# Optimization experiments

Measured on AMD Instinct MI355X. Metric: run time of the kernel, lower is better.

Reference implementation:

```python
import jax, jax.numpy as jnp
import numpy as np

HEADS = 4
DIM_HEAD = 128


def setup_inputs() -> dict:
    key = jax.random.key(0)
    k1, k2, k3, k4 = jax.random.split(key, 4)
    B, C, H, W = 8, 256, 64, 64
    hidden = HEADS * DIM_HEAD  # 512
    x = jax.random.normal(k1, (B, C, H, W), dtype=jnp.float32)
    # 1x1 convs are just channel matmuls; store kernels as [out_ch, in_ch]
    w_qkv = jax.random.normal(k2, (3 * hidden, C), dtype=jnp.float32) * 0.05
    w_out = jax.random.normal(k3, (C, hidden), dtype=jnp.float32) * 0.05
    b_out = jax.random.normal(k4, (C,), dtype=jnp.float32) * 0.05
    return {"x": x, "w_qkv": w_qkv, "w_out": w_out, "b_out": b_out}


def reference(x, w_qkv, w_out, b_out):
    B, C, H, W = x.shape
    n = H * W
    # to_qkv: 1x1 conv without bias == channel matmul
    qkv = jnp.einsum('bchw,oc->bohw', x, w_qkv)  # [B, 3*heads*dim_head, H, W]
    qkv = qkv.reshape(B, 3, HEADS, DIM_HEAD, n)  # 'b (qkv heads c) h w -> b qkv heads c n'
    q, k, v = qkv[:, 0], qkv[:, 1], qkv[:, 2]    # each [B, heads, dim_head, n]
    k = jax.nn.softmax(k, axis=-1)               # softmax over spatial positions
    context = jnp.einsum('bhdn,bhen->bhde', k, v)   # [B, heads, d, e]
    out = jnp.einsum('bhde,bhdn->bhen', context, q)  # [B, heads, e, n]
    out = out.reshape(B, HEADS * DIM_HEAD, H, W)
    # to_out: 1x1 conv with bias
    return jnp.einsum('bchw,oc->bohw', out, w_out) + b_out[None, :, None, None]
```

## Files before the change

kernel.cpp:

```cpp
#include <hip/hip_runtime.h>
#include <stdint.h>


using frag8 = __attribute__((ext_vector_type(8))) short;
using f32x4 = __attribute__((ext_vector_type(4))) float;

__device__ __forceinline__ unsigned short f2bf(float f) {
    union { float f; unsigned int u; } c; c.f = f;
    unsigned int u = c.u;
    return (unsigned short)((u + 0x7FFFu + ((u >> 16) & 1u)) >> 16);
}

__device__ __forceinline__ void gl_lds16(const void* g, void* l) {
    __builtin_amdgcn_global_load_lds(
        (const __attribute__((address_space(1))) unsigned int*)g,
        (__attribute__((address_space(3))) unsigned int*)l, 16, 0, 0);
}

__global__ __launch_bounds__(256) void k0_weights(
    const float* __restrict__ w_qkv, const float* __restrict__ w_out,
    unsigned short* __restrict__ wkvb, unsigned short* __restrict__ woutb,
    unsigned short* __restrict__ wqT)
{
    __shared__ float T[64][65];
    const int blk = blockIdx.x;
    const int tid = threadIdx.x;
    if (blk < 256) {
        const int idx = (blk * 256 + tid) * 4;
        float4 v = *(const float4*)(w_qkv + 512 * 256 + idx);
        ushort4 o;
        o.x = f2bf(v.x); o.y = f2bf(v.y); o.z = f2bf(v.z); o.w = f2bf(v.w);
        *(ushort4*)(wkvb + idx) = o;
    } else if (blk < 384) {
        const int idx = ((blk - 256) * 256 + tid) * 4;
        float4 v = *(const float4*)(w_out + idx);
        ushort4 o;
        o.x = f2bf(v.x); o.y = f2bf(v.y); o.z = f2bf(v.z); o.w = f2bf(v.w);
        *(ushort4*)(woutb + idx) = o;
    } else {
        const int t = blk - 384;
        const int j0 = (t >> 2) * 64, c0 = (t & 3) * 64;
        const int r = tid >> 4, cc = (tid & 15) * 4;
        #pragma unroll
        for (int p = 0; p < 4; ++p) {
            float4 v = *(const float4*)(w_qkv + (j0 + r + p * 16) * 256 + c0 + cc);
            T[r + p * 16][cc + 0] = v.x; T[r + p * 16][cc + 1] = v.y;
            T[r + p * 16][cc + 2] = v.z; T[r + p * 16][cc + 3] = v.w;
        }
        __syncthreads();
        const int c = tid >> 2, jj = (tid & 3) * 16;
        #pragma unroll
        for (int g = 0; g < 4; ++g) {
            ushort4 o;
            o.x = f2bf(T[jj + g * 4 + 0][c]);
            o.y = f2bf(T[jj + g * 4 + 1][c]);
            o.z = f2bf(T[jj + g * 4 + 2][c]);
            o.w = f2bf(T[jj + g * 4 + 3][c]);
            *(ushort4*)(wqT + (c0 + c) * 512 + j0 + jj + g * 4) = o;
        }
    }
}

__global__ __launch_bounds__(256) void k0_xt(
    const float* __restrict__ x, unsigned short* __restrict__ xbT)
{
    __shared__ float T[64][65];
    const int tid = threadIdx.x;
    const int n0 = blockIdx.x * 64, c0 = blockIdx.y * 64, b = blockIdx.z;
    const float* xb = x + (size_t)b * 1048576;
    const int cr = tid >> 4, nc = (tid & 15) * 4;
    #pragma unroll
    for (int p = 0; p < 4; ++p) {
        float4 v = *(const float4*)(xb + (size_t)(c0 + cr + p * 16) * 4096 + n0 + nc);
        T[cr + p * 16][nc + 0] = v.x; T[cr + p * 16][nc + 1] = v.y;
        T[cr + p * 16][nc + 2] = v.z; T[cr + p * 16][nc + 3] = v.w;
    }
    __syncthreads();
    const int n = tid >> 2, cc = (tid & 3) * 16;
    unsigned short* dst = xbT + (size_t)b * 1048576 + (size_t)(n0 + n) * 256 + c0 + cc;
    #pragma unroll
    for (int g = 0; g < 4; ++g) {
        ushort4 o;
        o.x = f2bf(T[cc + g * 4 + 0][n]);
        o.y = f2bf(T[cc + g * 4 + 1][n]);
        o.z = f2bf(T[cc + g * 4 + 2][n]);
        o.w = f2bf(T[cc + g * 4 + 3][n]);
        *(ushort4*)(dst + g * 4) = o;
    }
}

template<int MODE>
__global__ __launch_bounds__(256) void mfma_bt(
    const unsigned short* __restrict__ A0, int lda,
    const unsigned short* __restrict__ B0, int ldb,
    void* __restrict__ C0, int ldc,
    const float* __restrict__ bias, int Kp,
    unsigned long long sAz, unsigned long long sBz, unsigned long long sCz)
{
    __shared__ unsigned short As[128 * 32];
    __shared__ unsigned short Bs[128 * 32];
    const int tid  = threadIdx.x;
    const int w    = tid >> 6, lane = tid & 63;
    const int quad = lane >> 4, l16 = lane & 15;
    const int wm = (w >> 1) * 64, wn = (w & 1) * 64;
    const int z = blockIdx.z;

    const unsigned short* A;
    const unsigned short* B;
    int m0, n0;
    if constexpr (MODE == 3) {
        m0 = blockIdx.y * 128; n0 = 0;
        A = A0 + (unsigned long long)(z & 3) * 128ull + (unsigned long long)m0 * lda;
        B = B0 + (unsigned long long)z * 16384ull;
    } else {
        m0 = blockIdx.y * 128; n0 = blockIdx.x * 128;
        A = A0 + sAz * z + (unsigned long long)m0 * lda;
        B = B0 + sBz * z + (unsigned long long)n0 * ldb;
    }

    const int c0 = w * 128 + lane, c1 = c0 + 64;
    const int r0 = c0 >> 2, g0 = ((c0 & 3) ^ ((r0 >> 1) & 3)) * 8;
    const int r1 = c1 >> 2, g1 = ((c1 & 3) ^ ((r1 >> 1) & 3)) * 8;
    const unsigned short* gA0 = A + (unsigned long long)r0 * lda + g0;
    const unsigned short* gA1 = A + (unsigned long long)r1 * lda + g1;
    const unsigned short* gB0 = B + (unsigned long long)r0 * ldb + g0;
    const unsigned short* gB1 = B + (unsigned long long)r1 * ldb + g1;
    unsigned short* lA0 = As + w * 1024;
    unsigned short* lA1 = As + w * 1024 + 512;
    unsigned short* lB0 = Bs + w * 1024;
    unsigned short* lB1 = Bs + w * 1024 + 512;

    f32x4 acc[4][4] = {};

    for (int k0 = 0; k0 < Kp; k0 += 32) {
        gl_lds16(gA0 + k0, lA0);
        gl_lds16(gA1 + k0, lA1);
        gl_lds16(gB0 + k0, lB0);
        gl_lds16(gB1 + k0, lB1);
        __syncthreads();
        frag8 a[4], b[4];
        #pragma unroll
        for (int t = 0; t < 4; ++t) {
            const int ra = wm + t * 16 + l16;
            const int rb = wn + t * 16 + l16;
            a[t] = *(const frag8*)(As + ra * 32 + ((quad ^ ((ra >> 1) & 3)) << 3));
            b[t] = *(const frag8*)(Bs + rb * 32 + ((quad ^ ((rb >> 1) & 3)) << 3));
        }
        #pragma unroll
        for (int mt = 0; mt < 4; ++mt)
            #pragma unroll
            for (int nt = 0; nt < 4; ++nt)
                acc[mt][nt] = __builtin_amdgcn_mfma_f32_16x16x32_bf16(
                    a[mt], b[nt], acc[mt][nt], 0, 0, 0);
        __syncthreads();
    }

    if constexpr (MODE == 0 || MODE == 3) {
        unsigned short* C;
        if constexpr (MODE == 0)
            C = (unsigned short*)C0 + sCz * z + (unsigned long long)m0 * ldc + n0;
        else
            C = (unsigned short*)C0 + (unsigned long long)(z >> 2) * 131072ull
              + (unsigned long long)(z & 3) * 128ull + (unsigned long long)m0 * ldc;
        #pragma unroll
        for (int mt = 0; mt < 4; ++mt) {
            const int row = wm + mt * 16 + quad * 4;
            #pragma unroll
            for (int nt = 0; nt < 4; ++nt) {
                const int col = wn + nt * 16 + l16;
                #pragma unroll
                for (int r = 0; r < 4; ++r)
                    C[(unsigned long long)(row + r) * ldc + col] = f2bf(acc[mt][nt][r]);
            }
        }
    } else {
        float* C = (float*)C0 + sCz * z + (unsigned long long)m0 * ldc + n0;
        const float* bp = bias + m0;
        #pragma unroll
        for (int mt = 0; mt < 4; ++mt) {
            const int row = wm + mt * 16 + quad * 4;
            #pragma unroll
            for (int nt = 0; nt < 4; ++nt) {
                const int col = wn + nt * 16 + l16;
                #pragma unroll
                for (int r = 0; r < 4; ++r)
                    C[(unsigned long long)(row + r) * ldc + col] = acc[mt][nt][r] + bp[row + r];
            }
        }
    }
}

__global__ __launch_bounds__(256) void k13_ctx(
    const unsigned short* __restrict__ wkvb,
    const unsigned short* __restrict__ xbT,
    float* __restrict__ ctx, float* __restrict__ rowsum)
{
    __shared__ unsigned short As[128 * 32];
    __shared__ unsigned short Bs[128 * 32];
    __shared__ unsigned short Kt[128 * 128];
    __shared__ unsigned short Vt[128 * 128];
    const int tid  = threadIdx.x;
    const int w    = tid >> 6, lane = tid & 63;
    const int quad = lane >> 4, l16 = lane & 15;
    const int wm = (w >> 1) * 64, wn = (w & 1) * 64;
    const int s = blockIdx.x, h = blockIdx.y, b = blockIdx.z;

    const unsigned short* Wk = wkvb + (size_t)(h * 128) * 256;
    const unsigned short* Wv = wkvb + (size_t)(512 + h * 128) * 256;
    const unsigned short* Xb = xbT + (size_t)b * 1048576;

    const int c0 = w * 128 + lane, c1 = c0 + 64;
    const int r0 = c0 >> 2, g0 = ((c0 & 3) ^ ((r0 >> 1) & 3)) * 8;
    const int r1 = c1 >> 2, g1 = ((c1 & 3) ^ ((r1 >> 1) & 3)) * 8;
    unsigned short* lA0 = As + w * 1024;
    unsigned short* lA1 = As + w * 1024 + 512;
    unsigned short* lB0 = Bs + w * 1024;
    unsigned short* lB1 = Bs + w * 1024 + 512;

    float rsum[4][4] = {};
    f32x4 ctxa[4][4] = {};

    for (int ch = 0; ch < 2; ++ch) {
        const unsigned short* X0 = Xb + (size_t)(blockIdx.x * 256 + ch * 128) * 256;

        #pragma unroll 1
        for (int g = 0; g < 2; ++g) {
            const unsigned short* Wg = g ? Wv : Wk;
            f32x4 acc[4][4] = {};
            for (int k0 = 0; k0 < 256; k0 += 32) {
                gl_lds16(Wg + (size_t)r0 * 256 + g0 + k0, lA0);
                gl_lds16(Wg + (size_t)r1 * 256 + g1 + k0, lA1);
                gl_lds16(X0 + (size_t)r0 * 256 + g0 + k0, lB0);
                gl_lds16(X0 + (size_t)r1 * 256 + g1 + k0, lB1);
                __syncthreads();
                frag8 a[4], bb[4];
                #pragma unroll
                for (int t = 0; t < 4; ++t) {
                    const int ra = wm + t * 16 + l16;
                    const int rb = wn + t * 16 + l16;
                    a[t]  = *(const frag8*)(As + ra * 32 + ((quad ^ ((ra >> 1) & 3)) << 3));
                    bb[t] = *(const frag8*)(Bs + rb * 32 + ((quad ^ ((rb >> 1) & 3)) << 3));
                }
                #pragma unroll
                for (int mt = 0; mt < 4; ++mt)
                    #pragma unroll
                    for (int nt = 0; nt < 4; ++nt)
                        acc[mt][nt] = __builtin_amdgcn_mfma_f32_16x16x32_bf16(
                            a[mt], bb[nt], acc[mt][nt], 0, 0, 0);
                __syncthreads();
            }
            unsigned short* T = g ? Vt : Kt;
            if (g == 0) {
                #pragma unroll
                for (int mt = 0; mt < 4; ++mt) {
                    const int row = wm + mt * 16 + quad * 4;
                    #pragma unroll
                    for (int nt = 0; nt < 4; ++nt) {
                        const int col = wn + nt * 16 + l16;
                        #pragma unroll
                        for (int r = 0; r < 4; ++r) {
                            float e = __expf(acc[mt][nt][r]);
                            rsum[mt][r] += e;
                            T[((row + r) * 128 + col) ^ (((row + r) & 7) << 3)] = f2bf(e);
                        }
                    }
                }
            } else {
                #pragma unroll
                for (int mt = 0; mt < 4; ++mt) {
                    const int row = wm + mt * 16 + quad * 4;
                    #pragma unroll
                    for (int nt = 0; nt < 4; ++nt) {
                        const int col = wn + nt * 16 + l16;
                        #pragma unroll
                        for (int r = 0; r < 4; ++r)
                            T[((row + r) * 128 + col) ^ (((row + r) & 7) << 3)] =
                                f2bf(acc[mt][nt][r]);
                    }
                }
            }
        }
        __syncthreads();

        #pragma unroll
        for (int kk = 0; kk < 4; ++kk) {
            frag8 a[4], bb[4];
            #pragma unroll
            for (int t = 0; t < 4; ++t) {
                const int ra = wm + t * 16 + l16;
                const int rb = wn + t * 16 + l16;
                a[t]  = *(const frag8*)(Kt + ((ra * 128 + kk * 32 + quad * 8) ^ ((ra & 7) << 3)));
                bb[t] = *(const frag8*)(Vt + ((rb * 128 + kk * 32 + quad * 8) ^ ((rb & 7) << 3)));
            }
            #pragma unroll
            for (int mt = 0; mt < 4; ++mt)
                #pragma unroll
                for (int nt = 0; nt < 4; ++nt)
                    ctxa[mt][nt] = __builtin_amdgcn_mfma_f32_16x16x32_bf16(
                        a[mt], bb[nt], ctxa[mt][nt], 0, 0, 0);
        }
        __syncthreads();
    }

    float* cp = ctx + (size_t)(b * 4 + h) * 16384ull;
    #pragma unroll
    for (int mt = 0; mt < 4; ++mt) {
        const int row = wm + mt * 16 + quad * 4;
        #pragma unroll
        for (int nt = 0; nt < 4; ++nt) {
            const int col = wn + nt * 16 + l16;
            #pragma unroll
            for (int r = 0; r < 4; ++r)
                atomicAdd(cp + (row + r) * 128 + col, ctxa[mt][nt][r]);
        }
    }
    float* rs = rowsum + b * 512 + h * 128;
    #pragma unroll
    for (int mt = 0; mt < 4; ++mt) {
        const int row = wm + mt * 16 + quad * 4;
        #pragma unroll
        for (int r = 0; r < 4; ++r) {
            float v = rsum[mt][r];
            v += __shfl_xor(v, 1, 64);
            v += __shfl_xor(v, 2, 64);
            v += __shfl_xor(v, 4, 64);
            v += __shfl_xor(v, 8, 64);
            if (l16 == 0) atomicAdd(rs + row + r, v);
        }
    }
}

__global__ __launch_bounds__(256) void k3_scale(
    const float* __restrict__ ctx, const float* __restrict__ rowsum,
    unsigned short* __restrict__ ctxb)
{
    const int idx = (blockIdx.x * 256 + threadIdx.x) * 4;
    const float inv = 1.0f / rowsum[idx >> 7];
    float4 t = *(const float4*)(ctx + idx);
    ushort4 o;
    o.x = f2bf(t.x * inv); o.y = f2bf(t.y * inv);
    o.z = f2bf(t.z * inv); o.w = f2bf(t.w * inv);
    *(ushort4*)(ctxb + idx) = o;
}

extern "C" void kernel_launch(void* const* d_in, const int* in_sizes, int n_in,
                              void* d_out, int out_size, void* d_ws, size_t ws_size,
                              hipStream_t stream) {
    (void)in_sizes; (void)n_in; (void)out_size; (void)ws_size;
    const float* x     = (const float*)d_in[0];
    const float* w_qkv = (const float*)d_in[1];
    const float* w_out = (const float*)d_in[2];
    const float* b_out = (const float*)d_in[3];
    float* out = (float*)d_out;

    char* ws = (char*)d_ws;
    unsigned short* xbT    = (unsigned short*)ws;
    unsigned short* wkvb   = (unsigned short*)(ws + 16777216);
    unsigned short* woutb  = (unsigned short*)(ws + 17301504);
    unsigned short* wqT    = (unsigned short*)(ws + 17563648);
    float*          ctx    = (float*)(ws + 17825792);
    float*          rowsum = (float*)(ws + 19922944);
    unsigned short* ctxb   = (unsigned short*)(ws + 19939328);
    unsigned short* Mb     = (unsigned short*)(ws + 20987904);
    unsigned short* Nb     = (unsigned short*)(ws + 23085056);

    hipMemsetAsync(ws + 17825792, 0, 2097152 + 16384, stream);

    k0_weights<<<dim3(416), 256, 0, stream>>>(w_qkv, w_out, wkvb, woutb, wqT);
    k0_xt<<<dim3(64, 4, 8), 256, 0, stream>>>(x, xbT);
    k13_ctx<<<dim3(16, 4, 8), 256, 0, stream>>>(wkvb, xbT, ctx, rowsum);
    k3_scale<<<dim3(512), 256, 0, stream>>>(ctx, rowsum, ctxb);
    mfma_bt<3><<<dim3(1, 2, 32), 256, 0, stream>>>(
        woutb, 512, ctxb, 128, Mb, 512, nullptr, 128,
        0ull, 0ull, 0ull);
    mfma_bt<0><<<dim3(2, 2, 8), 256, 0, stream>>>(
        Mb, 512, wqT, 512, Nb, 256, nullptr, 512,
        131072ull, 0ull, 65536ull);
    mfma_bt<1><<<dim3(32, 2, 8), 256, 0, stream>>>(
        Nb, 256, xbT, 256, out, 4096, b_out, 256,
        65536ull, 1048576ull, 1048576ull);
}
```

Measured before the change: 200.5 us.

## Double-buffer K/V projection loads and fuse weight and x prep kernels

Merges the x-transpose and weight-conversion kernels into one launch to cut launch overhead. In the context kernel, K and V projections are computed together sharing the X fragment, with double-buffered global-to-LDS loads overlapped with MFMA through explicit waitcnt and barriers. LDS is unified into one 64KB buffer reused for staging and K/V tiles, and launch bounds request two blocks per CU. This raises register pressure because two accumulator sets are live at once, and it relies on hand-placed vmcnt counts being correct.

```diff
diff --git a/kernel.cpp b/kernel.cpp
--- a/kernel.cpp
+++ b/kernel.cpp
@@ -17,14 +17,40 @@
         (__attribute__((address_space(3))) unsigned int*)l, 16, 0, 0);
 }
 
-__global__ __launch_bounds__(256) void k0_weights(
-    const float* __restrict__ w_qkv, const float* __restrict__ w_out,
-    unsigned short* __restrict__ wkvb, unsigned short* __restrict__ woutb,
-    unsigned short* __restrict__ wqT)
+__global__ __launch_bounds__(256) void k0_prep(
+    const float* __restrict__ x, const float* __restrict__ w_qkv,
+    const float* __restrict__ w_out,
+    unsigned short* __restrict__ xbT, unsigned short* __restrict__ wkvb,
+    unsigned short* __restrict__ woutb, unsigned short* __restrict__ wqT)
 {
     __shared__ float T[64][65];
-    const int blk = blockIdx.x;
     const int tid = threadIdx.x;
+    const int blk0 = blockIdx.x;
+    if (blk0 < 2048) {
+        const int n0 = (blk0 & 63) * 64, c0 = ((blk0 >> 6) & 3) * 64, b = blk0 >> 8;
+        const float* xb = x + (size_t)b * 1048576;
+        const int cr = tid >> 4, nc = (tid & 15) * 4;
+        #pragma unroll
+        for (int p = 0; p < 4; ++p) {
+            float4 v = *(const float4*)(xb + (size_t)(c0 + cr + p * 16) * 4096 + n0 + nc);
+            T[cr + p * 16][nc + 0] = v.x; T[cr + p * 16][nc + 1] = v.y;
+            T[cr + p * 16][nc + 2] = v.z; T[cr + p * 16][nc + 3] = v.w;
+        }
+        __syncthreads();
+        const int n = tid >> 2, cc = (tid & 3) * 16;
+        unsigned short* dst = xbT + (size_t)b * 1048576 + (size_t)(n0 + n) * 256 + c0 + cc;
+        #pragma unroll
+        for (int g = 0; g < 4; ++g) {
+            ushort4 o;
+            o.x = f2bf(T[cc + g * 4 + 0][n]);
+            o.y = f2bf(T[cc + g * 4 + 1][n]);
+            o.z = f2bf(T[cc + g * 4 + 2][n]);
+            o.w = f2bf(T[cc + g * 4 + 3][n]);
+            *(ushort4*)(dst + g * 4) = o;
+        }
+        return;
+    }
+    const int blk = blk0 - 2048;
     if (blk < 256) {
         const int idx = (blk * 256 + tid) * 4;
         float4 v = *(const float4*)(w_qkv + 512 * 256 + idx);
@@ -61,34 +87,6 @@
     }
 }
 
-__global__ __launch_bounds__(256) void k0_xt(
-    const float* __restrict__ x, unsigned short* __restrict__ xbT)
-{
-    __shared__ float T[64][65];
-    const int tid = threadIdx.x;
-    const int n0 = blockIdx.x * 64, c0 = blockIdx.y * 64, b = blockIdx.z;
-    const float* xb = x + (size_t)b * 1048576;
-    const int cr = tid >> 4, nc = (tid & 15) * 4;
-    #pragma unroll
-    for (int p = 0; p < 4; ++p) {
-        float4 v = *(const float4*)(xb + (size_t)(c0 + cr + p * 16) * 4096 + n0 + nc);
-        T[cr + p * 16][nc + 0] = v.x; T[cr + p * 16][nc + 1] = v.y;
-        T[cr + p * 16][nc + 2] = v.z; T[cr + p * 16][nc + 3] = v.w;
-    }
-    __syncthreads();
-    const int n = tid >> 2, cc = (tid & 3) * 16;
-    unsigned short* dst = xbT + (size_t)b * 1048576 + (size_t)(n0 + n) * 256 + c0 + cc;
-    #pragma unroll
-    for (int g = 0; g < 4; ++g) {
-        ushort4 o;
-        o.x = f2bf(T[cc + g * 4 + 0][n]);
-        o.y = f2bf(T[cc + g * 4 + 1][n]);
-        o.z = f2bf(T[cc + g * 4 + 2][n]);
-        o.w = f2bf(T[cc + g * 4 + 3][n]);
-        *(ushort4*)(dst + g * 4) = o;
-    }
-}
-
 template<int MODE>
 __global__ __launch_bounds__(256) void mfma_bt(
     const unsigned short* __restrict__ A0, int lda,
@@ -190,93 +188,113 @@
     }
 }
 
-__global__ __launch_bounds__(256) void k13_ctx(
+__global__ __launch_bounds__(256, 2) void k13_ctx(
     const unsigned short* __restrict__ wkvb,
     const unsigned short* __restrict__ xbT,
     float* __restrict__ ctx, float* __restrict__ rowsum)
 {
-    __shared__ unsigned short As[128 * 32];
-    __shared__ unsigned short Bs[128 * 32];
-    __shared__ unsigned short Kt[128 * 128];
-    __shared__ unsigned short Vt[128 * 128];
+    __shared__ unsigned short smem[32768];
     const int tid  = threadIdx.x;
     const int w    = tid >> 6, lane = tid & 63;
     const int quad = lane >> 4, l16 = lane & 15;
     const int wm = (w >> 1) * 64, wn = (w & 1) * 64;
-    const int s = blockIdx.x, h = blockIdx.y, b = blockIdx.z;
+    const int h = blockIdx.y, b = blockIdx.z;
 
     const unsigned short* Wk = wkvb + (size_t)(h * 128) * 256;
     const unsigned short* Wv = wkvb + (size_t)(512 + h * 128) * 256;
-    const unsigned short* Xb = xbT + (size_t)b * 1048576;
+    const unsigned short* Xb = xbT + (size_t)b * 1048576 + (size_t)blockIdx.x * 65536;
 
     const int c0 = w * 128 + lane, c1 = c0 + 64;
-    const int r0 = c0 >> 2, g0 = ((c0 & 3) ^ ((r0 >> 1) & 3)) * 8;
-    const int r1 = c1 >> 2, g1 = ((c1 & 3) ^ ((r1 >> 1) & 3)) * 8;
-    unsigned short* lA0 = As + w * 1024;
-    unsigned short* lA1 = As + w * 1024 + 512;
-    unsigned short* lB0 = Bs + w * 1024;
-    unsigned short* lB1 = Bs + w * 1024 + 512;
+    const int r0 = c0 >> 2, s0 = ((c0 & 3) ^ ((r0 >> 1) & 3)) * 8;
+    const int r1 = c1 >> 2, s1 = ((c1 & 3) ^ ((r1 >> 1) & 3)) * 8;
+    const unsigned short* gWk0 = Wk + (size_t)r0 * 256 + s0;
+    const unsigned short* gWk1 = Wk + (size_t)r1 * 256 + s1;
+    const unsigned short* gWv0 = Wv + (size_t)r0 * 256 + s0;
+    const unsigned short* gWv1 = Wv + (size_t)r1 * 256 + s1;
+    const int ldsw = w * 1024;
+
+    unsigned short* Kt = smem;
+    unsigned short* Vt = smem + 16384;
 
     float rsum[4][4] = {};
     f32x4 ctxa[4][4] = {};
 
+    #pragma unroll 1
     for (int ch = 0; ch < 2; ++ch) {
-        const unsigned short* X0 = Xb + (size_t)(blockIdx.x * 256 + ch * 128) * 256;
-
-        #pragma unroll 1
-        for (int g = 0; g < 2; ++g) {
-            const unsigned short* Wg = g ? Wv : Wk;
-            f32x4 acc[4][4] = {};
-            for (int k0 = 0; k0 < 256; k0 += 32) {
-                gl_lds16(Wg + (size_t)r0 * 256 + g0 + k0, lA0);
-                gl_lds16(Wg + (size_t)r1 * 256 + g1 + k0, lA1);
-                gl_lds16(X0 + (size_t)r0 * 256 + g0 + k0, lB0);
-                gl_lds16(X0 + (size_t)r1 * 256 + g1 + k0, lB1);
-                __syncthreads();
-                frag8 a[4], bb[4];
-                #pragma unroll
-                for (int t = 0; t < 4; ++t) {
-                    const int ra = wm + t * 16 + l16;
-                    const int rb = wn + t * 16 + l16;
-                    a[t]  = *(const frag8*)(As + ra * 32 + ((quad ^ ((ra >> 1) & 3)) << 3));
-                    bb[t] = *(const frag8*)(Bs + rb * 32 + ((quad ^ ((rb >> 1) & 3)) << 3));
-                }
-                #pragma unroll
-                for (int mt = 0; mt < 4; ++mt)
-                    #pragma unroll
-                    for (int nt = 0; nt < 4; ++nt)
-                        acc[mt][nt] = __builtin_amdgcn_mfma_f32_16x16x32_bf16(
-                            a[mt], bb[nt], acc[mt][nt], 0, 0, 0);
-                __syncthreads();
-            }
-            unsigned short* T = g ? Vt : Kt;
-            if (g == 0) {
-                #pragma unroll
-                for (int mt = 0; mt < 4; ++mt) {
-                    const int row = wm + mt * 16 + quad * 4;
-                    #pragma unroll
-                    for (int nt = 0; nt < 4; ++nt) {
-                        const int col = wn + nt * 16 + l16;
-                        #pragma unroll
-                        for (int r = 0; r < 4; ++r) {
-                            float e = __expf(acc[mt][nt][r]);
-                            rsum[mt][r] += e;
-                            T[((row + r) * 128 + col) ^ (((row + r) & 7) << 3)] = f2bf(e);
-                        }
-                    }
-                }
+        const unsigned short* gX0 = Xb + (size_t)ch * 32768 + (size_t)r0 * 256 + s0;
+        const unsigned short* gX1 = Xb + (size_t)ch * 32768 + (size_t)r1 * 256 + s1;
+
+        f32x4 accK[4][4] = {};
+        f32x4 accV[4][4] = {};
+
+#define STAGE(T, BSEL) do {                                              \
+        unsigned short* bp_ = smem + (BSEL) * 12288 + ldsw;              \
+        gl_lds16(gWk0 + (T) * 32, bp_);                                  \
+        gl_lds16(gWk1 + (T) * 32, bp_ + 512);                            \
+        gl_lds16(gWv0 + (T) * 32, bp_ + 4096);                           \
+        gl_lds16(gWv1 + (T) * 32, bp_ + 4096 + 512);                     \
+        gl_lds16(gX0  + (T) * 32, bp_ + 8192);                           \
+        gl_lds16(gX1  + (T) * 32, bp_ + 8192 + 512);                     \
+    } while (0)
+
+        STAGE(0, 0);
+        #pragma unroll
+        for (int t = 0; t < 8; ++t) {
+            if (t < 7) {
+                STAGE(t + 1, (t + 1) & 1);
+                asm volatile("s_waitcnt vmcnt(6)" ::: "memory");
             } else {
-                #pragma unroll
-                for (int mt = 0; mt < 4; ++mt) {
-                    const int row = wm + mt * 16 + quad * 4;
-                    #pragma unroll
-                    for (int nt = 0; nt < 4; ++nt) {
-                        const int col = wn + nt * 16 + l16;
-                        #pragma unroll
-                        for (int r = 0; r < 4; ++r)
-                            T[((row + r) * 128 + col) ^ (((row + r) & 7) << 3)] =
-                                f2bf(acc[mt][nt][r]);
-                    }
+                asm volatile("s_waitcnt vmcnt(0)" ::: "memory");
+            }
+            __builtin_amdgcn_sched_barrier(0);
+            __builtin_amdgcn_s_barrier();
+            __builtin_amdgcn_sched_barrier(0);
+            const unsigned short* bp = smem + (t & 1) * 12288;
+            frag8 fb[4], fa[4];
+            #pragma unroll
+            for (int tt = 0; tt < 4; ++tt) {
+                const int rb = wn + tt * 16 + l16;
+                fb[tt] = *(const frag8*)(bp + 8192 + rb * 32 + ((quad ^ ((rb >> 1) & 3)) << 3));
+            }
+            #pragma unroll
+            for (int tt = 0; tt < 4; ++tt) {
+                const int ra = wm + tt * 16 + l16;
+                fa[tt] = *(const frag8*)(bp + ra * 32 + ((quad ^ ((ra >> 1) & 3)) << 3));
+            }
+            #pragma unroll
+            for (int mt = 0; mt < 4; ++mt)
+                #pragma unroll
+                for (int nt = 0; nt < 4; ++nt)
+                    accK[mt][nt] = __builtin_amdgcn_mfma_f32_16x16x32_bf16(
+                        fa[mt], fb[nt], accK[mt][nt], 0, 0, 0);
+            #pragma unroll
+            for (int tt = 0; tt < 4; ++tt) {
+                const int ra = wm + tt * 16 + l16;
+                fa[tt] = *(const frag8*)(bp + 4096 + ra * 32 + ((quad ^ ((ra >> 1) & 3)) << 3));
+            }
+            #pragma unroll
+            for (int mt = 0; mt < 4; ++mt)
+                #pragma unroll
+                for (int nt = 0; nt < 4; ++nt)
+                    accV[mt][nt] = __builtin_amdgcn_mfma_f32_16x16x32_bf16(
+                        fa[mt], fb[nt], accV[mt][nt], 0, 0, 0);
+            __builtin_amdgcn_sched_barrier(0);
+            __builtin_amdgcn_s_barrier();
+        }
+#undef STAGE
+
+        #pragma unroll
+        for (int mt = 0; mt < 4; ++mt) {
+            const int row = wm + mt * 16 + quad * 4;
+            #pragma unroll
+            for (int nt = 0; nt < 4; ++nt) {
+                const int col = wn + nt * 16 + l16;
+                #pragma unroll
+                for (int r = 0; r < 4; ++r) {
+                    float e = __expf(accK[mt][nt][r]);
+                    rsum[mt][r] += e;
+                    Kt[((row + r) * 128 + col) ^ (((row + r) & 7) << 3)] = f2bf(e);
+                    Vt[((row + r) * 128 + col) ^ (((row + r) & 7) << 3)] = f2bf(accV[mt][nt][r]);
                 }
             }
         }
@@ -366,8 +384,7 @@
 
     hipMemsetAsync(ws + 17825792, 0, 2097152 + 16384, stream);
 
-    k0_weights<<<dim3(416), 256, 0, stream>>>(w_qkv, w_out, wkvb, woutb, wqT);
-    k0_xt<<<dim3(64, 4, 8), 256, 0, stream>>>(x, xbT);
+    k0_prep<<<dim3(2464), 256, 0, stream>>>(x, w_qkv, w_out, xbT, wkvb, woutb, wqT);
     k13_ctx<<<dim3(16, 4, 8), 256, 0, stream>>>(wkvb, xbT, ctx, rowsum);
     k3_scale<<<dim3(512), 256, 0, stream>>>(ctx, rowsum, ctxb);
     mfma_bt<3><<<dim3(1, 2, 32), 256, 0, stream>>>(
```

New measurement: 240.7 us. 20.1% more time.
